# Kernel optimization log

Hardware: AMD Instinct MI355X
Metric: run time of the kernel (lower is better)

## Reference

```python
import jax, jax.numpy as jnp
import numpy as np

D_IN = 1024
D_OUT = 1024
NUM_HEADS = 16
HEAD_DIM = D_OUT // NUM_HEADS
B = 2
T = 2048


def setup_inputs() -> dict:
    key = jax.random.key(0)
    ks = jax.random.split(key, 6)
    scale = 0.02
    x = jax.random.normal(ks[0], (B, T, D_IN), dtype=jnp.float32)
    Wq = jax.random.normal(ks[1], (D_IN, D_OUT), dtype=jnp.float32) * scale
    Wk = jax.random.normal(ks[2], (D_IN, D_OUT), dtype=jnp.float32) * scale
    Wv = jax.random.normal(ks[3], (D_IN, D_OUT), dtype=jnp.float32) * scale
    Wo = jax.random.normal(ks[4], (D_OUT, D_OUT), dtype=jnp.float32) * scale
    bo = jax.random.normal(ks[5], (D_OUT,), dtype=jnp.float32) * scale
    key_padding_mask = jnp.zeros((B, T), dtype=bool)  # True = padded (masked out)
    return {"x": x, "Wq": Wq, "Wk": Wk, "Wv": Wv, "Wo": Wo, "bo": bo,
            "key_padding_mask": key_padding_mask}


def _mha(x, Wq, Wk, Wv, Wo, bo, key_padding_mask):
    b, t, _ = x.shape
    # projections then split heads: [b, t, H, hd] -> [b, H, t, hd]
    q = (x @ Wq).reshape(b, t, NUM_HEADS, HEAD_DIM).transpose(0, 2, 1, 3)
    k = (x @ Wk).reshape(b, t, NUM_HEADS, HEAD_DIM).transpose(0, 2, 1, 3)
    v = (x @ Wv).reshape(b, t, NUM_HEADS, HEAD_DIM).transpose(0, 2, 1, 3)
    # scores [b, H, t, t]
    scores = jnp.einsum('bhqd,bhkd->bhqk', q, k)
    neg_inf = jnp.float32(-jnp.inf)
    causal = jnp.triu(jnp.ones((t, t), dtype=bool), k=1)  # True above diagonal
    scores = jnp.where(causal[None, None, :, :], neg_inf, scores)
    scores = jnp.where(key_padding_mask[:, None, None, :], neg_inf, scores)
    attn = jax.nn.softmax(scores / np.sqrt(HEAD_DIM).astype(np.float32), axis=-1)
    # dropout p=0.0 -> identity
    ctx = jnp.einsum('bhqk,bhkd->bhqd', attn, v)  # [b, H, t, hd]
    ctx = ctx.transpose(0, 2, 1, 3).reshape(b, t, D_OUT)
    return ctx @ Wo + bo


def reference(x, Wq, Wk, Wv, Wo, bo, key_padding_mask):
    return _mha(x, Wq, Wk, Wv, Wo, bo, key_padding_mask)
```

## Files before the change

### kernel.cpp

```cpp
#include <hip/hip_runtime.h>
#include <math.h>

#define NHEAD 16
#define HD 64
#define BATCH 2
#define TSEQ 2048
#define MTOT (BATCH * TSEQ)
#define DDIM 1024
typedef unsigned short ushort_t;

using short8 = __attribute__((ext_vector_type(8))) short;
using f32x4  = __attribute__((ext_vector_type(4))) float;
using u32x4  = __attribute__((ext_vector_type(4))) unsigned int;
using u16x4  = __attribute__((ext_vector_type(4))) unsigned short;

#define QSCALE 0.18033688011112042f

static __device__ __forceinline__ ushort_t f2bf(float x) {
    unsigned int u = __builtin_bit_cast(unsigned int, x);
    u += 0x7fff + ((u >> 16) & 1);
    return (ushort_t)(u >> 16);
}

__global__ __launch_bounds__(256)
void convert_x_kernel(const float* __restrict__ X, ushort_t* __restrict__ Xb) {
    int i = (blockIdx.x * 256 + threadIdx.x) * 4;
    f32x4 v = *(const f32x4*)&X[i];
    u16x4 o;
    o.x = f2bf(v.x); o.y = f2bf(v.y); o.z = f2bf(v.z); o.w = f2bf(v.w);
    *(u16x4*)&Xb[i] = o;
}

__global__ __launch_bounds__(256)
void convert_wT_kernel(const float* __restrict__ Wq, const float* __restrict__ Wk,
                       const float* __restrict__ Wv, const float* __restrict__ Wo,
                       ushort_t* __restrict__ Wt) {
    int z = blockIdx.z;
    const float* W = (z == 0) ? Wq : (z == 1) ? Wk : (z == 2) ? Wv : Wo;
    ushort_t* dst = Wt + ((size_t)z << 20);
    __shared__ float tile[32][33];
    int r0 = blockIdx.y * 32, c0 = blockIdx.x * 32;
    int tx = threadIdx.x & 31, ty = threadIdx.x >> 5;
    #pragma unroll
    for (int i = 0; i < 4; ++i)
        tile[ty + i * 8][tx] = W[(size_t)(r0 + ty + i * 8) * DDIM + c0 + tx];
    __syncthreads();
    #pragma unroll
    for (int i = 0; i < 4; ++i)
        dst[(size_t)(c0 + ty + i * 8) * DDIM + r0 + tx] = f2bf(tile[tx][ty + i * 8]);
}

__global__ __launch_bounds__(256)
void qkv_gemm_kernel(const ushort_t* __restrict__ Xb, const ushort_t* __restrict__ Wt,
                     ushort_t* __restrict__ Qb, ushort_t* __restrict__ Kb,
                     ushort_t* __restrict__ Vt) {
    const int bx = blockIdx.x;
    const int z  = bx >> 3;
    const int n0 = (bx & 7) * 128;
    const int m0 = blockIdx.y * 128;
    const ushort_t* Wz = Wt + ((size_t)z << 20);

    __shared__ __align__(16) ushort_t As[128 * 32];
    __shared__ __align__(16) ushort_t Bs[128 * 32];

    const int tid = threadIdx.x;
    const int w = tid >> 6, l = tid & 63, ml = l & 15, q = l >> 4;
    const int wm = (w & 1) * 64, wn = (w >> 1) * 64;

    const int ci0 = tid, ci1 = tid + 256;
    const int ro0 = ci0 >> 2, co0 = (ci0 & 3) * 8;
    const int ro1 = ci1 >> 2, co1 = (ci1 & 3) * 8;
    const ushort_t* ap0 = Xb + (size_t)(m0 + ro0) * DDIM + co0;
    const ushort_t* ap1 = Xb + (size_t)(m0 + ro1) * DDIM + co1;
    const ushort_t* bp0 = Wz + (size_t)(n0 + ro0) * DDIM + co0;
    const ushort_t* bp1 = Wz + (size_t)(n0 + ro1) * DDIM + co1;

    f32x4 acc[4][4] = {};

    for (int k0 = 0; k0 < DDIM; k0 += 32) {
        u32x4 a0 = *(const u32x4*)(ap0 + k0);
        u32x4 a1 = *(const u32x4*)(ap1 + k0);
        u32x4 b0 = *(const u32x4*)(bp0 + k0);
        u32x4 b1 = *(const u32x4*)(bp1 + k0);
        __syncthreads();
        *(u32x4*)&As[ci0 * 8] = a0;  *(u32x4*)&As[ci1 * 8] = a1;
        *(u32x4*)&Bs[ci0 * 8] = b0;  *(u32x4*)&Bs[ci1 * 8] = b1;
        __syncthreads();
        short8 af[4], bfr[4];
        #pragma unroll
        for (int mi = 0; mi < 4; ++mi)
            af[mi] = *(const short8*)&As[(wm + mi * 16 + ml) * 32 + q * 8];
        #pragma unroll
        for (int ni = 0; ni < 4; ++ni)
            bfr[ni] = *(const short8*)&Bs[(wn + ni * 16 + ml) * 32 + q * 8];
        #pragma unroll
        for (int mi = 0; mi < 4; ++mi)
            #pragma unroll
            for (int ni = 0; ni < 4; ++ni)
                acc[mi][ni] = __builtin_amdgcn_mfma_f32_16x16x32_bf16(
                    af[mi], bfr[ni], acc[mi][ni], 0, 0, 0);
    }

    const float scale = (z == 0) ? QSCALE : 1.0f;
    #pragma unroll
    for (int mi = 0; mi < 4; ++mi) {
        #pragma unroll
        for (int ni = 0; ni < 4; ++ni) {
            #pragma unroll
            for (int r = 0; r < 4; ++r) {
                int mrow = m0 + wm + mi * 16 + q * 4 + r;
                int col  = n0 + wn + ni * 16 + ml;
                int b = mrow >> 11, t = mrow & 2047;
                int head = col >> 6, d = col & 63;
                size_t bh = (size_t)(b * NHEAD + head);
                ushort_t v = f2bf(acc[mi][ni][r] * scale);
                if (z == 0)      Qb[bh * 131072 + (size_t)t * 64 + d] = v;
                else if (z == 1) Kb[bh * 131072 + (size_t)t * 64 + d] = v;
                else             Vt[bh * 131072 + (size_t)d * 2048 + t] = v;
            }
        }
    }
}

__global__ __launch_bounds__(256)
void attn_kernel(const ushort_t* __restrict__ Qb, const ushort_t* __restrict__ Kb,
                 const ushort_t* __restrict__ Vt, ushort_t* __restrict__ ctx) {
    const int bh = blockIdx.y;
    const int pair = blockIdx.x;
    const int tid = threadIdx.x;
    const int w = tid >> 6, l = tid & 63, ml = l & 15, q = l >> 4;
    const size_t hb = (size_t)bh * 131072;

    __shared__ __align__(16) ushort_t Qs[4096];
    __shared__ __align__(16) ushort_t Ks[4096];
    __shared__ __align__(16) ushort_t Vs[4096];
    __shared__ __align__(16) ushort_t Ps[4096];

    const int ci0 = tid, ci1 = tid + 256;
    const int s0 = ci0 >> 8, r0 = (ci0 & 255) >> 2, c0 = (ci0 & 3) * 8;
    const int s1 = ci1 >> 8, r1 = (ci1 & 255) >> 2, c1 = (ci1 & 3) * 8;

    for (int half = 0; half < 2; ++half) {
        const int qt = half ? (31 - pair) : pair;
        const int q0 = qt * 64;

        u32x4 qv0 = *(const u32x4*)(Qb + hb + (size_t)(q0 + r0) * 64 + s0 * 32 + c0);
        u32x4 qv1 = *(const u32x4*)(Qb + hb + (size_t)(q0 + r1) * 64 + s1 * 32 + c1);
        __syncthreads();
        *(u32x4*)&Qs[ci0 * 8] = qv0;
        *(u32x4*)&Qs[ci1 * 8] = qv1;

        f32x4 o[4] = {};
        float m_i[4] = {-INFINITY, -INFINITY, -INFINITY, -INFINITY};
        float l_i[4] = {};
        short8 aQ0, aQ1;

        for (int nt = 0; nt <= qt; ++nt) {
            const int n0 = nt * 64;
            u32x4 kv0 = *(const u32x4*)(Kb + hb + (size_t)(n0 + r0) * 64 + s0 * 32 + c0);
            u32x4 kv1 = *(const u32x4*)(Kb + hb + (size_t)(n0 + r1) * 64 + s1 * 32 + c1);
            u32x4 vv0 = *(const u32x4*)(Vt + hb + (size_t)r0 * 2048 + n0 + s0 * 32 + c0);
            u32x4 vv1 = *(const u32x4*)(Vt + hb + (size_t)r1 * 2048 + n0 + s1 * 32 + c1);
            __syncthreads();
            *(u32x4*)&Ks[ci0 * 8] = kv0;  *(u32x4*)&Ks[ci1 * 8] = kv1;
            *(u32x4*)&Vs[ci0 * 8] = vv0;  *(u32x4*)&Vs[ci1 * 8] = vv1;
            __syncthreads();

            if (nt == 0) {
                aQ0 = *(const short8*)&Qs[(w * 16 + ml) * 32 + q * 8];
                aQ1 = *(const short8*)&Qs[2048 + (w * 16 + ml) * 32 + q * 8];
            }

            f32x4 s[4];
            #pragma unroll
            for (int tn = 0; tn < 4; ++tn) {
                short8 b0 = *(const short8*)&Ks[(tn * 16 + ml) * 32 + q * 8];
                short8 b1 = *(const short8*)&Ks[2048 + (tn * 16 + ml) * 32 + q * 8];
                f32x4 zz = {};
                zz = __builtin_amdgcn_mfma_f32_16x16x32_bf16(aQ0, b0, zz, 0, 0, 0);
                zz = __builtin_amdgcn_mfma_f32_16x16x32_bf16(aQ1, b1, zz, 0, 0, 0);
                s[tn] = zz;
            }

            if (nt == qt) {
                #pragma unroll
                for (int tn = 0; tn < 4; ++tn)
                    #pragma unroll
                    for (int r = 0; r < 4; ++r)
                        if (tn * 16 + ml > w * 16 + q * 4 + r) s[tn][r] = -INFINITY;
            }

            float alpha[4];
            #pragma unroll
            for (int r = 0; r < 4; ++r) {
                float mx = fmaxf(fmaxf(s[0][r], s[1][r]), fmaxf(s[2][r], s[3][r]));
                mx = fmaxf(mx, __shfl_xor(mx, 1));
                mx = fmaxf(mx, __shfl_xor(mx, 2));
                mx = fmaxf(mx, __shfl_xor(mx, 4));
                mx = fmaxf(mx, __shfl_xor(mx, 8));
                float mnew = fmaxf(m_i[r], mx);
                alpha[r] = exp2f(m_i[r] - mnew);
                m_i[r] = mnew;
                float rs = 0.f;
                #pragma unroll
                for (int tn = 0; tn < 4; ++tn) {
                    float p = exp2f(s[tn][r] - mnew);
                    s[tn][r] = p;
                    rs += p;
                }
                rs += __shfl_xor(rs, 1);
                rs += __shfl_xor(rs, 2);
                rs += __shfl_xor(rs, 4);
                rs += __shfl_xor(rs, 8);
                l_i[r] = l_i[r] * alpha[r] + rs;
            }
            #pragma unroll
            for (int tn = 0; tn < 4; ++tn) {
                o[tn][0] *= alpha[0]; o[tn][1] *= alpha[1];
                o[tn][2] *= alpha[2]; o[tn][3] *= alpha[3];
            }

            #pragma unroll
            for (int tn = 0; tn < 4; ++tn) {
                int c = tn * 16 + ml;
                #pragma unroll
                for (int r = 0; r < 4; ++r)
                    Ps[w * 1024 + (c >> 5) * 512 + (q * 4 + r) * 32 + (c & 31)] =
                        f2bf(s[tn][r]);
            }

            #pragma unroll
            for (int ss = 0; ss < 2; ++ss) {
                short8 aP = *(const short8*)&Ps[w * 1024 + ss * 512 + ml * 32 + q * 8];
                #pragma unroll
                for (int tn = 0; tn < 4; ++tn) {
                    short8 bV = *(const short8*)&Vs[ss * 2048 + (tn * 16 + ml) * 32 + q * 8];
                    o[tn] = __builtin_amdgcn_mfma_f32_16x16x32_bf16(aP, bV, o[tn], 0, 0, 0);
                }
            }
        }

        const int b = bh >> 4, h = bh & 15;
        #pragma unroll
        for (int r = 0; r < 4; ++r) {
            float inv = 1.0f / l_i[r];
            int t = q0 + w * 16 + q * 4 + r;
            size_t mrow = (size_t)(b * TSEQ + t) * DDIM;
            #pragma unroll
            for (int tn = 0; tn < 4; ++tn)
                ctx[mrow + h * 64 + tn * 16 + ml] = f2bf(o[tn][r] * inv);
        }
    }
}

__global__ __launch_bounds__(256)
void out_gemm_kernel(const ushort_t* __restrict__ Cx, const ushort_t* __restrict__ Wt,
                     const float* __restrict__ bo, float* __restrict__ out) {
    const int n0 = blockIdx.x * 128;
    const int m0 = blockIdx.y * 128;
    const ushort_t* Wz = Wt + ((size_t)3 << 20);

    __shared__ __align__(16) ushort_t As[128 * 32];
    __shared__ __align__(16) ushort_t Bs[128 * 32];

    const int tid = threadIdx.x;
    const int w = tid >> 6, l = tid & 63, ml = l & 15, q = l >> 4;
    const int wm = (w & 1) * 64, wn = (w >> 1) * 64;

    const int ci0 = tid, ci1 = tid + 256;
    const int ro0 = ci0 >> 2, co0 = (ci0 & 3) * 8;
    const int ro1 = ci1 >> 2, co1 = (ci1 & 3) * 8;
    const ushort_t* ap0 = Cx + (size_t)(m0 + ro0) * DDIM + co0;
    const ushort_t* ap1 = Cx + (size_t)(m0 + ro1) * DDIM + co1;
    const ushort_t* bp0 = Wz + (size_t)(n0 + ro0) * DDIM + co0;
    const ushort_t* bp1 = Wz + (size_t)(n0 + ro1) * DDIM + co1;

    f32x4 acc[4][4] = {};

    for (int k0 = 0; k0 < DDIM; k0 += 32) {
        u32x4 a0 = *(const u32x4*)(ap0 + k0);
        u32x4 a1 = *(const u32x4*)(ap1 + k0);
        u32x4 b0 = *(const u32x4*)(bp0 + k0);
        u32x4 b1 = *(const u32x4*)(bp1 + k0);
        __syncthreads();
        *(u32x4*)&As[ci0 * 8] = a0;  *(u32x4*)&As[ci1 * 8] = a1;
        *(u32x4*)&Bs[ci0 * 8] = b0;  *(u32x4*)&Bs[ci1 * 8] = b1;
        __syncthreads();
        short8 af[4], bfr[4];
        #pragma unroll
        for (int mi = 0; mi < 4; ++mi)
            af[mi] = *(const short8*)&As[(wm + mi * 16 + ml) * 32 + q * 8];
        #pragma unroll
        for (int ni = 0; ni < 4; ++ni)
            bfr[ni] = *(const short8*)&Bs[(wn + ni * 16 + ml) * 32 + q * 8];
        #pragma unroll
        for (int mi = 0; mi < 4; ++mi)
            #pragma unroll
            for (int ni = 0; ni < 4; ++ni)
                acc[mi][ni] = __builtin_amdgcn_mfma_f32_16x16x32_bf16(
                    af[mi], bfr[ni], acc[mi][ni], 0, 0, 0);
    }

    #pragma unroll
    for (int mi = 0; mi < 4; ++mi) {
        #pragma unroll
        for (int ni = 0; ni < 4; ++ni) {
            int col = n0 + wn + ni * 16 + ml;
            float bias = bo[col];
            #pragma unroll
            for (int r = 0; r < 4; ++r) {
                int mrow = m0 + wm + mi * 16 + q * 4 + r;
                out[(size_t)mrow * DDIM + col] = acc[mi][ni][r] + bias;
            }
        }
    }
}

extern "C" void kernel_launch(void* const* d_in, const int* in_sizes, int n_in,
                              void* d_out, int out_size, void* d_ws, size_t ws_size,
                              hipStream_t stream)
{
    const float* x  = (const float*)d_in[0];
    const float* Wq = (const float*)d_in[1];
    const float* Wk = (const float*)d_in[2];
    const float* Wv = (const float*)d_in[3];
    const float* Wo = (const float*)d_in[4];
    const float* bo = (const float*)d_in[5];

    char* ws = (char*)d_ws;
    ushort_t* Xb  = (ushort_t*)(ws);
    ushort_t* Wt  = (ushort_t*)(ws + (8u  << 20));
    ushort_t* Qb  = (ushort_t*)(ws + (16u << 20));
    ushort_t* Kb  = (ushort_t*)(ws + (24u << 20));
    ushort_t* Vt  = (ushort_t*)(ws + (32u << 20));
    ushort_t* Cx  = (ushort_t*)(ws + (40u << 20));

    convert_x_kernel<<<dim3(MTOT * DDIM / 1024), 256, 0, stream>>>(x, Xb);
    convert_wT_kernel<<<dim3(32, 32, 4), 256, 0, stream>>>(Wq, Wk, Wv, Wo, Wt);
    qkv_gemm_kernel<<<dim3(24, 32), 256, 0, stream>>>(Xb, Wt, Qb, Kb, Vt);
    attn_kernel<<<dim3(16, 32), 256, 0, stream>>>(Qb, Kb, Vt, Cx);
    out_gemm_kernel<<<dim3(8, 32), 256, 0, stream>>>(Cx, Wt, bo, (float*)d_out);
}
```

Measured before the change: 232.7 us.

## Restructure attention to 128-row query blocks with transposed MFMA and padded LDS

```diff
diff --git a/kernel.cpp b/kernel.cpp
--- a/kernel.cpp
+++ b/kernel.cpp
@@ -122,133 +122,156 @@
     }
 }
 
-__global__ __launch_bounds__(256)
+__global__ __launch_bounds__(256, 3)
 void attn_kernel(const ushort_t* __restrict__ Qb, const ushort_t* __restrict__ Kb,
                  const ushort_t* __restrict__ Vt, ushort_t* __restrict__ ctx) {
-    const int bh = blockIdx.y;
-    const int pair = blockIdx.x;
+    const int qtB = 15 - blockIdx.x;
+    const int bh  = blockIdx.y;
+    const int q0b = qtB * 128;
     const int tid = threadIdx.x;
-    const int w = tid >> 6, l = tid & 63, ml = l & 15, q = l >> 4;
+    const int w = tid >> 6, l = tid & 63, ml = l & 15, quad = l >> 4;
     const size_t hb = (size_t)bh * 131072;
 
-    __shared__ __align__(16) ushort_t Qs[4096];
-    __shared__ __align__(16) ushort_t Ks[4096];
-    __shared__ __align__(16) ushort_t Vs[4096];
-    __shared__ __align__(16) ushort_t Ps[4096];
-
-    const int ci0 = tid, ci1 = tid + 256;
-    const int s0 = ci0 >> 8, r0 = (ci0 & 255) >> 2, c0 = (ci0 & 3) * 8;
-    const int s1 = ci1 >> 8, r1 = (ci1 & 255) >> 2, c1 = (ci1 & 3) * 8;
-
-    for (int half = 0; half < 2; ++half) {
-        const int qt = half ? (31 - pair) : pair;
-        const int q0 = qt * 64;
-
-        u32x4 qv0 = *(const u32x4*)(Qb + hb + (size_t)(q0 + r0) * 64 + s0 * 32 + c0);
-        u32x4 qv1 = *(const u32x4*)(Qb + hb + (size_t)(q0 + r1) * 64 + s1 * 32 + c1);
-        __syncthreads();
-        *(u32x4*)&Qs[ci0 * 8] = qv0;
-        *(u32x4*)&Qs[ci1 * 8] = qv1;
-
-        f32x4 o[4] = {};
-        float m_i[4] = {-INFINITY, -INFINITY, -INFINITY, -INFINITY};
-        float l_i[4] = {};
-        short8 aQ0, aQ1;
-
-        for (int nt = 0; nt <= qt; ++nt) {
-            const int n0 = nt * 64;
-            u32x4 kv0 = *(const u32x4*)(Kb + hb + (size_t)(n0 + r0) * 64 + s0 * 32 + c0);
-            u32x4 kv1 = *(const u32x4*)(Kb + hb + (size_t)(n0 + r1) * 64 + s1 * 32 + c1);
-            u32x4 vv0 = *(const u32x4*)(Vt + hb + (size_t)r0 * 2048 + n0 + s0 * 32 + c0);
-            u32x4 vv1 = *(const u32x4*)(Vt + hb + (size_t)r1 * 2048 + n0 + s1 * 32 + c1);
-            __syncthreads();
-            *(u32x4*)&Ks[ci0 * 8] = kv0;  *(u32x4*)&Ks[ci1 * 8] = kv1;
-            *(u32x4*)&Vs[ci0 * 8] = vv0;  *(u32x4*)&Vs[ci1 * 8] = vv1;
-            __syncthreads();
-
-            if (nt == 0) {
-                aQ0 = *(const short8*)&Qs[(w * 16 + ml) * 32 + q * 8];
-                aQ1 = *(const short8*)&Qs[2048 + (w * 16 + ml) * 32 + q * 8];
-            }
-
-            f32x4 s[4];
-            #pragma unroll
-            for (int tn = 0; tn < 4; ++tn) {
-                short8 b0 = *(const short8*)&Ks[(tn * 16 + ml) * 32 + q * 8];
-                short8 b1 = *(const short8*)&Ks[2048 + (tn * 16 + ml) * 32 + q * 8];
-                f32x4 zz = {};
-                zz = __builtin_amdgcn_mfma_f32_16x16x32_bf16(aQ0, b0, zz, 0, 0, 0);
-                zz = __builtin_amdgcn_mfma_f32_16x16x32_bf16(aQ1, b1, zz, 0, 0, 0);
-                s[tn] = zz;
-            }
-
-            if (nt == qt) {
-                #pragma unroll
-                for (int tn = 0; tn < 4; ++tn)
+    __shared__ __align__(16) ushort_t Ks[64 * 72];
+    __shared__ __align__(16) ushort_t Vs[64 * 72];
+    __shared__ __align__(16) ushort_t Ps[4 * 32 * 72];
+
+    const int q0w = q0b + w * 32;
+    ushort_t* PsW = Ps + w * (32 * 72);
+
+    short8 bQ[2][2];
+    #pragma unroll
+    for (int qn = 0; qn < 2; ++qn)
+        #pragma unroll
+        for (int ss = 0; ss < 2; ++ss)
+            bQ[qn][ss] = *(const short8*)(Qb + hb +
+                (size_t)(q0w + qn * 16 + ml) * 64 + ss * 32 + quad * 8);
+
+    f32x4 o[4][2] = {};
+    float m_i[2] = {-INFINITY, -INFINITY};
+    float l_i[2] = {0.f, 0.f};
+
+    const int c0 = tid, c1 = tid + 256;
+    const int r0 = c0 >> 3, h0 = c0 & 7;
+    const int r1 = c1 >> 3, h1 = c1 & 7;
+
+    const int nTiles = qtB * 2 + 2;
+
+    for (int nt = 0; nt < nTiles; ++nt) {
+        const int n0 = nt * 64;
+        u32x4 kv0 = *(const u32x4*)(Kb + hb + (size_t)(n0 + r0) * 64 + h0 * 8);
+        u32x4 kv1 = *(const u32x4*)(Kb + hb + (size_t)(n0 + r1) * 64 + h1 * 8);
+        u32x4 vv0 = *(const u32x4*)(Vt + hb + (size_t)r0 * 2048 + n0 + h0 * 8);
+        u32x4 vv1 = *(const u32x4*)(Vt + hb + (size_t)r1 * 2048 + n0 + h1 * 8);
+        __syncthreads();
+        *(u32x4*)&Ks[r0 * 72 + h0 * 8] = kv0;
+        *(u32x4*)&Ks[r1 * 72 + h1 * 8] = kv1;
+        *(u32x4*)&Vs[r0 * 72 + h0 * 8] = vv0;
+        *(u32x4*)&Vs[r1 * 72 + h1 * 8] = vv1;
+        __syncthreads();
+
+        if (n0 <= q0w + 31) {
+            f32x4 s[2][4];
+            #pragma unroll
+            for (int tk = 0; tk < 4; ++tk) {
+                short8 aK0 = *(const short8*)&Ks[(tk * 16 + ml) * 72 + quad * 8];
+                short8 aK1 = *(const short8*)&Ks[(tk * 16 + ml) * 72 + 32 + quad * 8];
+                #pragma unroll
+                for (int qn = 0; qn < 2; ++qn) {
+                    f32x4 zz = {};
+                    zz = __builtin_amdgcn_mfma_f32_16x16x32_bf16(aK0, bQ[qn][0], zz, 0, 0, 0);
+                    zz = __builtin_amdgcn_mfma_f32_16x16x32_bf16(aK1, bQ[qn][1], zz, 0, 0, 0);
+                    s[qn][tk] = zz;
+                }
+            }
+
+            if (n0 + 63 > q0w) {
+                #pragma unroll
+                for (int qn = 0; qn < 2; ++qn) {
+                    int qrow = q0w + qn * 16 + ml;
                     #pragma unroll
-                    for (int r = 0; r < 4; ++r)
-                        if (tn * 16 + ml > w * 16 + q * 4 + r) s[tn][r] = -INFINITY;
-            }
-
-            float alpha[4];
-            #pragma unroll
-            for (int r = 0; r < 4; ++r) {
-                float mx = fmaxf(fmaxf(s[0][r], s[1][r]), fmaxf(s[2][r], s[3][r]));
-                mx = fmaxf(mx, __shfl_xor(mx, 1));
-                mx = fmaxf(mx, __shfl_xor(mx, 2));
-                mx = fmaxf(mx, __shfl_xor(mx, 4));
-                mx = fmaxf(mx, __shfl_xor(mx, 8));
-                float mnew = fmaxf(m_i[r], mx);
-                alpha[r] = exp2f(m_i[r] - mnew);
-                m_i[r] = mnew;
+                    for (int tk = 0; tk < 4; ++tk)
+                        #pragma unroll
+                        for (int r = 0; r < 4; ++r)
+                            if (n0 + tk * 16 + quad * 4 + r > qrow)
+                                s[qn][tk][r] = -INFINITY;
+                }
+            }
+
+            float alpha[2];
+            #pragma unroll
+            for (int qn = 0; qn < 2; ++qn) {
+                f32x4 mm;
+                #pragma unroll
+                for (int e = 0; e < 4; ++e)
+                    mm[e] = fmaxf(fmaxf(s[qn][0][e], s[qn][1][e]),
+                                  fmaxf(s[qn][2][e], s[qn][3][e]));
+                float mx = fmaxf(fmaxf(mm[0], mm[1]), fmaxf(mm[2], mm[3]));
+                mx = fmaxf(mx, __shfl_xor(mx, 16));
+                mx = fmaxf(mx, __shfl_xor(mx, 32));
+                float mnew = fmaxf(m_i[qn], mx);
+                alpha[qn] = exp2f(m_i[qn] - mnew);
+                m_i[qn] = mnew;
                 float rs = 0.f;
                 #pragma unroll
-                for (int tn = 0; tn < 4; ++tn) {
-                    float p = exp2f(s[tn][r] - mnew);
-                    s[tn][r] = p;
-                    rs += p;
+                for (int tk = 0; tk < 4; ++tk)
+                    #pragma unroll
+                    for (int r = 0; r < 4; ++r) {
+                        float p = exp2f(s[qn][tk][r] - mnew);
+                        s[qn][tk][r] = p;
+                        rs += p;
+                    }
+                rs += __shfl_xor(rs, 16);
+                rs += __shfl_xor(rs, 32);
+                l_i[qn] = l_i[qn] * alpha[qn] + rs;
+            }
+
+            #pragma unroll
+            for (int td = 0; td < 4; ++td) {
+                o[td][0] *= alpha[0];
+                o[td][1] *= alpha[1];
+            }
+
+            #pragma unroll
+            for (int qn = 0; qn < 2; ++qn)
+                #pragma unroll
+                for (int tk = 0; tk < 4; ++tk) {
+                    u16x4 pk;
+                    pk.x = f2bf(s[qn][tk][0]);
+                    pk.y = f2bf(s[qn][tk][1]);
+                    pk.z = f2bf(s[qn][tk][2]);
+                    pk.w = f2bf(s[qn][tk][3]);
+                    *(u16x4*)&PsW[(qn * 16 + ml) * 72 + tk * 16 + quad * 4] = pk;
                 }
-                rs += __shfl_xor(rs, 1);
-                rs += __shfl_xor(rs, 2);
-                rs += __shfl_xor(rs, 4);
-                rs += __shfl_xor(rs, 8);
-                l_i[r] = l_i[r] * alpha[r] + rs;
-            }
-            #pragma unroll
-            for (int tn = 0; tn < 4; ++tn) {
-                o[tn][0] *= alpha[0]; o[tn][1] *= alpha[1];
-                o[tn][2] *= alpha[2]; o[tn][3] *= alpha[3];
-            }
-
-            #pragma unroll
-            for (int tn = 0; tn < 4; ++tn) {
-                int c = tn * 16 + ml;
-                #pragma unroll
-                for (int r = 0; r < 4; ++r)
-                    Ps[w * 1024 + (c >> 5) * 512 + (q * 4 + r) * 32 + (c & 31)] =
-                        f2bf(s[tn][r]);
-            }
 
             #pragma unroll
             for (int ss = 0; ss < 2; ++ss) {
-                short8 aP = *(const short8*)&Ps[w * 1024 + ss * 512 + ml * 32 + q * 8];
-                #pragma unroll
-                for (int tn = 0; tn < 4; ++tn) {
-                    short8 bV = *(const short8*)&Vs[ss * 2048 + (tn * 16 + ml) * 32 + q * 8];
-                    o[tn] = __builtin_amdgcn_mfma_f32_16x16x32_bf16(aP, bV, o[tn], 0, 0, 0);
+                short8 bP0 = *(const short8*)&PsW[ml * 72 + ss * 32 + quad * 8];
+                short8 bP1 = *(const short8*)&PsW[(16 + ml) * 72 + ss * 32 + quad * 8];
+                #pragma unroll
+                for (int td = 0; td < 4; ++td) {
+                    short8 aV = *(const short8*)&Vs[(td * 16 + ml) * 72 + ss * 32 + quad * 8];
+                    o[td][0] = __builtin_amdgcn_mfma_f32_16x16x32_bf16(aV, bP0, o[td][0], 0, 0, 0);
+                    o[td][1] = __builtin_amdgcn_mfma_f32_16x16x32_bf16(aV, bP1, o[td][1], 0, 0, 0);
                 }
             }
         }
-
-        const int b = bh >> 4, h = bh & 15;
-        #pragma unroll
-        for (int r = 0; r < 4; ++r) {
-            float inv = 1.0f / l_i[r];
-            int t = q0 + w * 16 + q * 4 + r;
-            size_t mrow = (size_t)(b * TSEQ + t) * DDIM;
-            #pragma unroll
-            for (int tn = 0; tn < 4; ++tn)
-                ctx[mrow + h * 64 + tn * 16 + ml] = f2bf(o[tn][r] * inv);
+    }
+
+    const int b = bh >> 4, h = bh & 15;
+    #pragma unroll
+    for (int qn = 0; qn < 2; ++qn) {
+        float inv = 1.0f / l_i[qn];
+        int t = q0w + qn * 16 + ml;
+        size_t rowb = ((size_t)(b * TSEQ + t)) * DDIM + h * 64;
+        #pragma unroll
+        for (int td = 0; td < 4; ++td) {
+            u16x4 pk;
+            pk.x = f2bf(o[td][qn][0] * inv);
+            pk.y = f2bf(o[td][qn][1] * inv);
+            pk.z = f2bf(o[td][qn][2] * inv);
+            pk.w = f2bf(o[td][qn][3] * inv);
+            *(u16x4*)&ctx[rowb + td * 16 + quad * 4] = pk;
         }
     }
 }
```

New measurement: 240.3 us. 1.03x slower.
